# Performance work log

Hardware: AMD Instinct MI355X
Metric: run time of the kernel (lower is better)

## Reference

```python
import jax, jax.numpy as jnp
import numpy as np

NUM_HEADS = 16
THRESHOLD = 4e-4  # < 1/S so every softmax row keeps >=1 entry (classical path of grover_search_filter)


def setup_inputs() -> dict:
    key = jax.random.key(0)
    k0, k1, k2 = jax.random.split(key, 3)
    B, S, E = 4, 1024, 1024
    x = jax.random.normal(k0, (B, S, E), dtype=jnp.float32)
    Wqkv = jax.random.normal(k1, (3 * E, E), dtype=jnp.float32) * 0.02
    bqkv = jnp.zeros((3 * E,), dtype=jnp.float32)
    Wproj = jax.random.normal(k2, (E, E), dtype=jnp.float32) * 0.02
    bproj = jnp.zeros((E,), dtype=jnp.float32)
    return {"x": x, "Wqkv": Wqkv, "bqkv": bqkv, "Wproj": Wproj, "bproj": bproj}


def reference(x, Wqkv, bqkv, Wproj, bproj):
    B, S, E = x.shape
    H = NUM_HEADS
    D = E // H
    scale = D ** -0.5
    # qkv projection -> (3, B, H, S, D), matching torch permute(2,0,3,1,4)
    qkv = (x @ Wqkv.T + bqkv).reshape(B, S, 3, H, D).transpose(2, 0, 3, 1, 4)
    q, k, v = qkv[0], qkv[1], qkv[2]
    attn_logits = jnp.einsum("bhqd,bhkd->bhqk", q, k) * scale  # [B,H,S,S]
    attn_probs = jax.nn.softmax(attn_logits, axis=-1)
    # grover_search_filter: seq_len > 2**max_qubits -> classical threshold mask
    selected = attn_probs > THRESHOLD
    filtered_logits = jnp.where(selected, attn_logits, -jnp.inf)
    filtered_attn = jax.nn.softmax(filtered_logits, axis=-1)
    # dropout is identity in eval mode
    out = jnp.einsum("bhqk,bhkd->bhqd", filtered_attn, v)
    out = out.transpose(0, 2, 1, 3).reshape(B, S, E)
    out = out @ Wproj.T + bproj
    return out, filtered_attn
```

## Files before the change

kernel.cpp:

```cpp
#include <hip/hip_runtime.h>
#include <hip/hip_bf16.h>
#include <cstdint>


#define BB 4
#define SS 1024
#define EE 1024
#define HH 16
#define DD 64

typedef __attribute__((ext_vector_type(8))) short bf16x8;
typedef __attribute__((ext_vector_type(4))) float f32x4;

__global__ __launch_bounds__(256) void split_f32(
    const float* __restrict__ in, __hip_bfloat16* __restrict__ hi,
    __hip_bfloat16* __restrict__ lo, int n4) {
  int i = blockIdx.x * 256 + threadIdx.x;
  if (i >= n4) return;
  float4 v = ((const float4*)in)[i];
  float vv[4] = {v.x, v.y, v.z, v.w};
  __hip_bfloat16 h[4], l[4];
#pragma unroll
  for (int j = 0; j < 4; ++j) {
    h[j] = __float2bfloat16(vv[j]);
    l[j] = __float2bfloat16(vv[j] - __bfloat162float(h[j]));
  }
  ((ushort4*)hi)[i] = *(ushort4*)h;
  if (lo) ((ushort4*)lo)[i] = *(ushort4*)l;
}

template <int MODE>
__global__ __launch_bounds__(256) void gemm(
    const __hip_bfloat16* __restrict__ Ah, const __hip_bfloat16* __restrict__ Al,
    const __hip_bfloat16* __restrict__ Bh, const __hip_bfloat16* __restrict__ Bl,
    const float* __restrict__ Af, const float* __restrict__ bias,
    float* __restrict__ oF, __hip_bfloat16* __restrict__ o1,
    __hip_bfloat16* __restrict__ o2, __hip_bfloat16* __restrict__ o3,
    __hip_bfloat16* __restrict__ o4, __hip_bfloat16* __restrict__ o5,
    int M, int N, int K, int lda, int ldb, long long sA, long long sB) {
  constexpr bool SPLIT = (MODE == 0 || MODE == 1);
  constexpr bool AF32  = (MODE == 2);

  const int tid  = threadIdx.x;
  const int lane = tid & 63;
  const int wave = tid >> 6;
  const int wm   = (wave >> 1) * 64;
  const int wn   = (wave & 1) * 64;
  const int quad = lane >> 4;
  const int l15  = lane & 15;
  const int m0   = blockIdx.y * 128;
  const int n0   = blockIdx.x * 128;
  const long long zz = blockIdx.z;

  if (AF32) Af += zz * sA;
  else { Ah += zz * sA; if (SPLIT) Al += zz * sA; }
  Bh += zz * sB;
  if (SPLIT) Bl += zz * sB;

  __shared__ __align__(16) __hip_bfloat16 lds[(SPLIT ? 4 : 2) * 128 * 72];
  __hip_bfloat16* lAh = lds;
  __hip_bfloat16* lAl = SPLIT ? lds + 128 * 72 : nullptr;
  __hip_bfloat16* lBh = lds + (SPLIT ? 2 : 1) * 128 * 72;
  __hip_bfloat16* lBl = SPLIT ? lds + 3 * 128 * 72 : nullptr;

  f32x4 acc[4][4] = {};

  for (int k0 = 0; k0 < K; k0 += 64) {
#pragma unroll
    for (int it = 0; it < 4; ++it) {
      int flat = (it * 256 + tid) * 8;
      int row  = flat >> 6;
      int kk   = flat & 63;
      const bool mok = (m0 + row < M);
      const bool nok = (n0 + row < N);
      if (AF32) {
        float4 f0 = {0, 0, 0, 0}, f1 = {0, 0, 0, 0};
        if (mok) {
          const float* src = Af + (long long)(m0 + row) * lda + k0 + kk;
          f0 = *(const float4*)src;
          f1 = *(const float4*)(src + 4);
        }
        __hip_bfloat16 t[8];
        t[0] = __float2bfloat16(f0.x); t[1] = __float2bfloat16(f0.y);
        t[2] = __float2bfloat16(f0.z); t[3] = __float2bfloat16(f0.w);
        t[4] = __float2bfloat16(f1.x); t[5] = __float2bfloat16(f1.y);
        t[6] = __float2bfloat16(f1.z); t[7] = __float2bfloat16(f1.w);
        *(uint4*)&lAh[row * 72 + kk] = *(uint4*)t;
      } else {
        uint4 va = {0, 0, 0, 0};
        if (mok) va = *(const uint4*)(Ah + (long long)(m0 + row) * lda + k0 + kk);
        *(uint4*)&lAh[row * 72 + kk] = va;
        if (SPLIT) {
          uint4 vl = {0, 0, 0, 0};
          if (mok) vl = *(const uint4*)(Al + (long long)(m0 + row) * lda + k0 + kk);
          *(uint4*)&lAl[row * 72 + kk] = vl;
        }
      }
      uint4 vb = {0, 0, 0, 0};
      if (nok) vb = *(const uint4*)(Bh + (long long)(n0 + row) * ldb + k0 + kk);
      *(uint4*)&lBh[row * 72 + kk] = vb;
      if (SPLIT) {
        uint4 vbl = {0, 0, 0, 0};
        if (nok) vbl = *(const uint4*)(Bl + (long long)(n0 + row) * ldb + k0 + kk);
        *(uint4*)&lBl[row * 72 + kk] = vbl;
      }
    }
    __syncthreads();

#pragma unroll
    for (int ks = 0; ks < 64; ks += 32) {
      bf16x8 ah[4], bh[4], al[4], bl[4];
#pragma unroll
      for (int i = 0; i < 4; ++i) {
        int off = (wm + i * 16 + l15) * 72 + ks + quad * 8;
        ah[i] = *(const bf16x8*)&lAh[off];
        if (SPLIT) al[i] = *(const bf16x8*)&lAl[off];
      }
#pragma unroll
      for (int j = 0; j < 4; ++j) {
        int off = (wn + j * 16 + l15) * 72 + ks + quad * 8;
        bh[j] = *(const bf16x8*)&lBh[off];
        if (SPLIT) bl[j] = *(const bf16x8*)&lBl[off];
      }
#pragma unroll
      for (int i = 0; i < 4; ++i)
#pragma unroll
        for (int j = 0; j < 4; ++j) {
          if (SPLIT) {
            acc[i][j] = __builtin_amdgcn_mfma_f32_16x16x32_bf16(al[i], bh[j], acc[i][j], 0, 0, 0);
            acc[i][j] = __builtin_amdgcn_mfma_f32_16x16x32_bf16(ah[i], bl[j], acc[i][j], 0, 0, 0);
          }
          acc[i][j] = __builtin_amdgcn_mfma_f32_16x16x32_bf16(ah[i], bh[j], acc[i][j], 0, 0, 0);
        }
    }
    __syncthreads();
  }

#pragma unroll
  for (int i = 0; i < 4; ++i) {
#pragma unroll
    for (int j = 0; j < 4; ++j) {
#pragma unroll
      for (int r = 0; r < 4; ++r) {
        int m = m0 + wm + i * 16 + quad * 4 + r;
        int n = n0 + wn + j * 16 + l15;
        float v = acc[i][j][r];
        if (MODE == 0) {
          v += bias[n];
          int c = n >> 10, nn = n & 1023, h = nn >> 6, d = nn & 63;
          int b = m >> 10, s = m & 1023;
          long long idx = (((long long)(b * HH + h) * SS + s) << 6) + d;
          if (c == 0) {
            v *= 0.125f;
            __hip_bfloat16 hh = __float2bfloat16(v);
            o1[idx] = hh;
            o2[idx] = __float2bfloat16(v - __bfloat162float(hh));
          } else if (c == 1) {
            __hip_bfloat16 hh = __float2bfloat16(v);
            o3[idx] = hh;
            o4[idx] = __float2bfloat16(v - __bfloat162float(hh));
          } else {
            o5[(((long long)(b * HH + h) * DD + d) << 10) + s] = __float2bfloat16(v);
          }
        } else if (MODE == 1) {
          oF[zz * (SS * SS) + (long long)m * SS + n] = v * 0.125f;
        } else if (MODE == 2) {
          if (n < DD) {
            int b = (int)(zz >> 4), h = (int)(zz & 15);
            o1[(((long long)(b * SS + m)) << 10) + h * DD + n] = __float2bfloat16(v);
          }
        } else {
          oF[(long long)m * EE + n] = v + bias[n];
        }
      }
    }
  }
}

__device__ __forceinline__ float qg_max16(float v) {
#pragma unroll
  for (int o = 8; o > 0; o >>= 1) v = fmaxf(v, __shfl_xor(v, o));
  return v;
}
__device__ __forceinline__ float qg_sum16(float v) {
#pragma unroll
  for (int o = 8; o > 0; o >>= 1) v += __shfl_xor(v, o);
  return v;
}

__global__ __launch_bounds__(512, 4) void fused_attn(
    const __hip_bfloat16* __restrict__ qh, const __hip_bfloat16* __restrict__ ql,
    const __hip_bfloat16* __restrict__ kh, const __hip_bfloat16* __restrict__ kl,
    const __hip_bfloat16* __restrict__ vT, float* __restrict__ attn,
    __hip_bfloat16* __restrict__ ao) {
  const int tid  = threadIdx.x;
  const int lane = tid & 63;
  const int wave = tid >> 6;
  const int quad = lane >> 4;
  const int l15  = lane & 15;

  int id = blockIdx.x;
  const int q8 = gridDim.x >> 3;
  id = (id & 7) * q8 + (id >> 3);
  const int bh = id >> 5;
  const int q0 = (id & 31) * 32;

  const int brow = (bh >> 4) * SS;
  const int h    = bh & 15;
  const long long qbase = ((long long)bh * SS + q0) * DD;
  const long long kbase = (long long)bh * SS * DD;
  const long long vbase = (long long)bh * DD * SS;
  const long long abase = ((long long)bh * SS + q0) * SS;

  __shared__ __align__(16) __hip_bfloat16 Pl[32][1032];
  __shared__ float red[3][8][32];
  __shared__ float Obuf[4][32][17];

  bf16x8 aqh0[2], aqh1[2], aql0[2], aql1[2];
#pragma unroll
  for (int s = 0; s < 2; ++s) {
    const __hip_bfloat16* ph = qh + qbase + (s * 16 + l15) * DD + quad * 8;
    const __hip_bfloat16* pl = ql + qbase + (s * 16 + l15) * DD + quad * 8;
    aqh0[s] = *(const bf16x8*)(ph);
    aqh1[s] = *(const bf16x8*)(ph + 32);
    aql0[s] = *(const bf16x8*)(pl);
    aql1[s] = *(const bf16x8*)(pl + 32);
  }

  f32x4 acc0[8], acc1[8];
  const __hip_bfloat16* pkh0 = kh + kbase + (long long)(wave * 128 + l15) * DD + quad * 8;
  const __hip_bfloat16* pkl0 = kl + kbase + (long long)(wave * 128 + l15) * DD + quad * 8;
#pragma unroll
  for (int nt = 0; nt < 8; ++nt) {
    const __hip_bfloat16* pkh = pkh0 + nt * 16 * DD;
    const __hip_bfloat16* pkl = pkl0 + nt * 16 * DD;
    f32x4 a0 = {}, a1 = {};
    {
      bf16x8 b = *(const bf16x8*)(pkh);
      bf16x8 c = *(const bf16x8*)(pkl);
      __builtin_amdgcn_s_setprio(1);
      a0 = __builtin_amdgcn_mfma_f32_16x16x32_bf16(aql0[0], b, a0, 0, 0, 0);
      a1 = __builtin_amdgcn_mfma_f32_16x16x32_bf16(aql0[1], b, a1, 0, 0, 0);
      a0 = __builtin_amdgcn_mfma_f32_16x16x32_bf16(aqh0[0], c, a0, 0, 0, 0);
      a1 = __builtin_amdgcn_mfma_f32_16x16x32_bf16(aqh0[1], c, a1, 0, 0, 0);
      a0 = __builtin_amdgcn_mfma_f32_16x16x32_bf16(aqh0[0], b, a0, 0, 0, 0);
      a1 = __builtin_amdgcn_mfma_f32_16x16x32_bf16(aqh0[1], b, a1, 0, 0, 0);
      __builtin_amdgcn_s_setprio(0);
    }
    {
      bf16x8 b = *(const bf16x8*)(pkh + 32);
      bf16x8 c = *(const bf16x8*)(pkl + 32);
      __builtin_amdgcn_s_setprio(1);
      a0 = __builtin_amdgcn_mfma_f32_16x16x32_bf16(aql1[0], b, a0, 0, 0, 0);
      a1 = __builtin_amdgcn_mfma_f32_16x16x32_bf16(aql1[1], b, a1, 0, 0, 0);
      a0 = __builtin_amdgcn_mfma_f32_16x16x32_bf16(aqh1[0], c, a0, 0, 0, 0);
      a1 = __builtin_amdgcn_mfma_f32_16x16x32_bf16(aqh1[1], c, a1, 0, 0, 0);
      a0 = __builtin_amdgcn_mfma_f32_16x16x32_bf16(aqh1[0], b, a0, 0, 0, 0);
      a1 = __builtin_amdgcn_mfma_f32_16x16x32_bf16(aqh1[1], b, a1, 0, 0, 0);
      __builtin_amdgcn_s_setprio(0);
    }
    acc0[nt] = a0;
    acc1[nt] = a1;
  }

  {
    float mx0[4], mx1[4];
#pragma unroll
    for (int r = 0; r < 4; ++r) {
      float a = fmaxf(fmaxf(fmaxf(acc0[0][r], acc0[1][r]), fmaxf(acc0[2][r], acc0[3][r])),
                      fmaxf(fmaxf(acc0[4][r], acc0[5][r]), fmaxf(acc0[6][r], acc0[7][r])));
      mx0[r] = qg_max16(a);
      float b = fmaxf(fmaxf(fmaxf(acc1[0][r], acc1[1][r]), fmaxf(acc1[2][r], acc1[3][r])),
                      fmaxf(fmaxf(acc1[4][r], acc1[5][r]), fmaxf(acc1[6][r], acc1[7][r])));
      mx1[r] = qg_max16(b);
    }
    if (l15 == 0) {
#pragma unroll
      for (int r = 0; r < 4; ++r) {
        red[0][wave][quad * 4 + r]      = mx0[r];
        red[0][wave][16 + quad * 4 + r] = mx1[r];
      }
    }
  }
  __syncthreads();
  float m0[4], m1[4];
#pragma unroll
  for (int r = 0; r < 4; ++r) {
    const int q = quad * 4 + r;
    m0[r] = fmaxf(fmaxf(fmaxf(red[0][0][q], red[0][1][q]), fmaxf(red[0][2][q], red[0][3][q])),
                  fmaxf(fmaxf(red[0][4][q], red[0][5][q]), fmaxf(red[0][6][q], red[0][7][q])));
    m1[r] = fmaxf(fmaxf(fmaxf(red[0][0][16 + q], red[0][1][16 + q]), fmaxf(red[0][2][16 + q], red[0][3][16 + q])),
                  fmaxf(fmaxf(red[0][4][16 + q], red[0][5][16 + q]), fmaxf(red[0][6][16 + q], red[0][7][16 + q])));
  }

  {
    float z0[4] = {0.f, 0.f, 0.f, 0.f}, z1[4] = {0.f, 0.f, 0.f, 0.f};
#pragma unroll
    for (int nt = 0; nt < 8; ++nt)
#pragma unroll
      for (int r = 0; r < 4; ++r) {
        float e0 = expf(acc0[nt][r] - m0[r]);
        acc0[nt][r] = e0; z0[r] += e0;
        float e1 = expf(acc1[nt][r] - m1[r]);
        acc1[nt][r] = e1; z1[r] += e1;
      }
#pragma unroll
    for (int r = 0; r < 4; ++r) { z0[r] = qg_sum16(z0[r]); z1[r] = qg_sum16(z1[r]); }
    if (l15 == 0) {
#pragma unroll
      for (int r = 0; r < 4; ++r) {
        red[1][wave][quad * 4 + r]      = z0[r];
        red[1][wave][16 + quad * 4 + r] = z1[r];
      }
    }
  }
  __syncthreads();
  float c0[4], c1[4];
#pragma unroll
  for (int r = 0; r < 4; ++r) {
    const int q = quad * 4 + r;
    const float Z0 = ((red[1][0][q] + red[1][1][q]) + (red[1][2][q] + red[1][3][q])) +
                     ((red[1][4][q] + red[1][5][q]) + (red[1][6][q] + red[1][7][q]));
    const float Z1 = ((red[1][0][16 + q] + red[1][1][16 + q]) + (red[1][2][16 + q] + red[1][3][16 + q])) +
                     ((red[1][4][16 + q] + red[1][5][16 + q]) + (red[1][6][16 + q] + red[1][7][16 + q]));
    c0[r] = 4e-4f * Z0;
    c1[r] = 4e-4f * Z1;
  }

  {
    float s0[4] = {0.f, 0.f, 0.f, 0.f}, s1[4] = {0.f, 0.f, 0.f, 0.f};
#pragma unroll
    for (int nt = 0; nt < 8; ++nt)
#pragma unroll
      for (int r = 0; r < 4; ++r) {
        if (acc0[nt][r] > c0[r]) s0[r] += acc0[nt][r];
        if (acc1[nt][r] > c1[r]) s1[r] += acc1[nt][r];
      }
#pragma unroll
    for (int r = 0; r < 4; ++r) { s0[r] = qg_sum16(s0[r]); s1[r] = qg_sum16(s1[r]); }
    if (l15 == 0) {
#pragma unroll
      for (int r = 0; r < 4; ++r) {
        red[2][wave][quad * 4 + r]      = s0[r];
        red[2][wave][16 + quad * 4 + r] = s1[r];
      }
    }
  }
  __syncthreads();
  float rinv0[4], rinv1[4];
#pragma unroll
  for (int r = 0; r < 4; ++r) {
    const int q = quad * 4 + r;
    const float Zs0 = ((red[2][0][q] + red[2][1][q]) + (red[2][2][q] + red[2][3][q])) +
                      ((red[2][4][q] + red[2][5][q]) + (red[2][6][q] + red[2][7][q]));
    const float Zs1 = ((red[2][0][16 + q] + red[2][1][16 + q]) + (red[2][2][16 + q] + red[2][3][16 + q])) +
                      ((red[2][4][16 + q] + red[2][5][16 + q]) + (red[2][6][16 + q] + red[2][7][16 + q]));
    rinv0[r] = 1.0f / Zs0;
    rinv1[r] = 1.0f / Zs1;
  }

#pragma unroll
  for (int nt = 0; nt < 8; ++nt) {
    const int k = wave * 128 + nt * 16 + l15;
#pragma unroll
    for (int r = 0; r < 4; ++r) {
      const int q = quad * 4 + r;
      const float e0 = acc0[nt][r];
      const float p0 = (e0 > c0[r]) ? e0 * rinv0[r] : 0.f;
      attn[abase + (long long)q * SS + k] = p0;
      Pl[q][k] = __float2bfloat16(p0);
      const float e1 = acc1[nt][r];
      const float p1 = (e1 > c1[r]) ? e1 * rinv1[r] : 0.f;
      attn[abase + (long long)(16 + q) * SS + k] = p1;
      Pl[16 + q][k] = __float2bfloat16(p1);
    }
  }
  __syncthreads();

  const int d0  = (wave & 3) * 16;
  const int kh2 = (wave >> 2) * 512;
  f32x4 oA0 = {}, oA1 = {}, oB0 = {}, oB1 = {};
  const __hip_bfloat16* pv  = vT + vbase + (long long)(d0 + l15) * SS + kh2 + quad * 8;
  const __hip_bfloat16* pp0 = &Pl[l15][kh2] + quad * 8;
  const __hip_bfloat16* pp1 = &Pl[16 + l15][kh2] + quad * 8;
#pragma unroll
  for (int ks = 0; ks < 16; ks += 2) {
    bf16x8 v0  = *(const bf16x8*)(pv + ks * 32);
    bf16x8 v1  = *(const bf16x8*)(pv + (ks + 1) * 32);
    bf16x8 a00 = *(const bf16x8*)(pp0 + ks * 32);
    bf16x8 a01 = *(const bf16x8*)(pp0 + (ks + 1) * 32);
    bf16x8 a10 = *(const bf16x8*)(pp1 + ks * 32);
    bf16x8 a11 = *(const bf16x8*)(pp1 + (ks + 1) * 32);
    __builtin_amdgcn_s_setprio(1);
    oA0 = __builtin_amdgcn_mfma_f32_16x16x32_bf16(a00, v0, oA0, 0, 0, 0);
    oB0 = __builtin_amdgcn_mfma_f32_16x16x32_bf16(a10, v0, oB0, 0, 0, 0);
    oA1 = __builtin_amdgcn_mfma_f32_16x16x32_bf16(a01, v1, oA1, 0, 0, 0);
    oB1 = __builtin_amdgcn_mfma_f32_16x16x32_bf16(a11, v1, oB1, 0, 0, 0);
    __builtin_amdgcn_s_setprio(0);
  }
  float oS0[4], oS1[4];
#pragma unroll
  for (int r = 0; r < 4; ++r) { oS0[r] = oA0[r] + oA1[r]; oS1[r] = oB0[r] + oB1[r]; }

  if (wave >= 4) {
#pragma unroll
    for (int r = 0; r < 4; ++r) {
      Obuf[wave & 3][quad * 4 + r][l15]      = oS0[r];
      Obuf[wave & 3][16 + quad * 4 + r][l15] = oS1[r];
    }
  }
  __syncthreads();
  if (wave < 4) {
#pragma unroll
    for (int r = 0; r < 4; ++r) {
      const int qA = q0 + quad * 4 + r;
      const int qB = qA + 16;
      const float vA = oS0[r] + Obuf[wave][quad * 4 + r][l15];
      const float vB = oS1[r] + Obuf[wave][16 + quad * 4 + r][l15];
      ao[((long long)(brow + qA)) * EE + h * DD + d0 + l15] = __float2bfloat16(vA);
      ao[((long long)(brow + qB)) * EE + h * DD + d0 + l15] = __float2bfloat16(vB);
    }
  }
}

extern "C" void kernel_launch(void* const* d_in, const int* in_sizes, int n_in,
                              void* d_out, int out_size, void* d_ws, size_t ws_size,
                              hipStream_t stream) {
  const float* x     = (const float*)d_in[0];
  const float* Wqkv  = (const float*)d_in[1];
  const float* bqkv  = (const float*)d_in[2];
  const float* Wproj = (const float*)d_in[3];
  const float* bproj = (const float*)d_in[4];

  float* out   = (float*)d_out;
  float* attnF = out + (size_t)BB * SS * EE;

  const size_t M1 = 1024 * 1024;
  __hip_bfloat16* w = (__hip_bfloat16*)d_ws;

  if (ws_size >= (size_t)80 * 1024 * 1024) {
    __hip_bfloat16 *xh = w, *xl = xh + 4 * M1;
    __hip_bfloat16 *Wqh = xl + 4 * M1, *Wql = Wqh + 3 * M1, *Wph = Wql + 3 * M1;
    __hip_bfloat16 *qh = Wph + M1, *ql = qh + 4 * M1, *kh = ql + 4 * M1, *kl = kh + 4 * M1;
    __hip_bfloat16 *vT = kl + 4 * M1, *ao = vT + 4 * M1;

    split_f32<<<4096, 256, 0, stream>>>(x, xh, xl, 1024 * 1024);
    split_f32<<<3072, 256, 0, stream>>>(Wqkv, Wqh, Wql, 768 * 1024);
    split_f32<<<1024, 256, 0, stream>>>(Wproj, Wph, nullptr, 256 * 1024);

    gemm<0><<<dim3(24, 32, 1), 256, 0, stream>>>(
        xh, xl, Wqh, Wql, nullptr, bqkv, nullptr, qh, ql, kh, kl, vT,
        4096, 3072, 1024, 1024, 1024, 0LL, 0LL);
    fused_attn<<<dim3(BB * HH * 32), 512, 0, stream>>>(
        qh, ql, kh, kl, vT, attnF, ao);
    gemm<3><<<dim3(8, 32, 1), 256, 0, stream>>>(
        ao, nullptr, Wph, nullptr, nullptr, bproj, out, nullptr, nullptr, nullptr, nullptr, nullptr,
        4096, 1024, 1024, 1024, 1024, 0LL, 0LL);
    return;
  }

  __hip_bfloat16 *Wqh = w, *Wql = Wqh + 3 * M1, *Wph = Wql + 3 * M1;
  __hip_bfloat16 *xh = Wph + M1, *xl = xh + M1;
  __hip_bfloat16 *qh = xl + M1, *ql = qh + M1, *kh = ql + M1, *kl = kh + M1;
  __hip_bfloat16 *vT = kl + M1, *ao = vT + M1;

  split_f32<<<3072, 256, 0, stream>>>(Wqkv, Wqh, Wql, 768 * 1024);
  split_f32<<<1024, 256, 0, stream>>>(Wproj, Wph, nullptr, 256 * 1024);

  for (int b = 0; b < BB; ++b) {
    const float* xb   = x + (size_t)b * SS * EE;
    float* attnb      = attnF + (size_t)b * HH * SS * SS;
    float* outb       = out + (size_t)b * SS * EE;

    split_f32<<<1024, 256, 0, stream>>>(xb, xh, xl, 256 * 1024);
    gemm<0><<<dim3(24, 8, 1), 256, 0, stream>>>(
        xh, xl, Wqh, Wql, nullptr, bqkv, nullptr, qh, ql, kh, kl, vT,
        1024, 3072, 1024, 1024, 1024, 0LL, 0LL);
    fused_attn<<<dim3(HH * 32), 512, 0, stream>>>(
        qh, ql, kh, kl, vT, attnb, ao);
    gemm<3><<<dim3(8, 8, 1), 256, 0, stream>>>(
        ao, nullptr, Wph, nullptr, nullptr, bproj, outb, nullptr, nullptr, nullptr, nullptr, nullptr,
        1024, 1024, 1024, 1024, 1024, 0LL, 0LL);
  }
}
```

Before: 670.4 us.

## Fuse x bf16 split into QKV GEMM and merge weight split kernels

The QKV GEMM now reads fp32 x directly and splits it into hi/lo bf16 while staging tiles into LDS. This removes the separate split pass and its 16 MB of hi/lo bf16 intermediates for x. The weight operands are no longer staged through LDS and are loaded straight from global memory into registers, and the two weight split kernels are merged into one launch. The direct B loads are strided per lane and uncoalesced, and they are re-read by each wave, which may raise memory traffic in exchange for less LDS use.

After: 649.9 us. 3.1% less time.

```diff
diff --git a/kernel.cpp b/kernel.cpp
--- a/kernel.cpp
+++ b/kernel.cpp
@@ -12,35 +12,39 @@
 typedef __attribute__((ext_vector_type(8))) short bf16x8;
 typedef __attribute__((ext_vector_type(4))) float f32x4;
 
-__global__ __launch_bounds__(256) void split_f32(
-    const float* __restrict__ in, __hip_bfloat16* __restrict__ hi,
-    __hip_bfloat16* __restrict__ lo, int n4) {
+__global__ __launch_bounds__(256) void split_w(
+    const float* __restrict__ Wqkv, const float* __restrict__ Wproj,
+    __hip_bfloat16* __restrict__ Wqh, __hip_bfloat16* __restrict__ Wql,
+    __hip_bfloat16* __restrict__ Wph) {
   int i = blockIdx.x * 256 + threadIdx.x;
-  if (i >= n4) return;
-  float4 v = ((const float4*)in)[i];
-  float vv[4] = {v.x, v.y, v.z, v.w};
-  __hip_bfloat16 h[4], l[4];
-#pragma unroll
-  for (int j = 0; j < 4; ++j) {
-    h[j] = __float2bfloat16(vv[j]);
-    l[j] = __float2bfloat16(vv[j] - __bfloat162float(h[j]));
-  }
-  ((ushort4*)hi)[i] = *(ushort4*)h;
-  if (lo) ((ushort4*)lo)[i] = *(ushort4*)l;
-}
-
-template <int MODE>
-__global__ __launch_bounds__(256) void gemm(
-    const __hip_bfloat16* __restrict__ Ah, const __hip_bfloat16* __restrict__ Al,
-    const __hip_bfloat16* __restrict__ Bh, const __hip_bfloat16* __restrict__ Bl,
-    const float* __restrict__ Af, const float* __restrict__ bias,
-    float* __restrict__ oF, __hip_bfloat16* __restrict__ o1,
-    __hip_bfloat16* __restrict__ o2, __hip_bfloat16* __restrict__ o3,
-    __hip_bfloat16* __restrict__ o4, __hip_bfloat16* __restrict__ o5,
-    int M, int N, int K, int lda, int ldb, long long sA, long long sB) {
-  constexpr bool SPLIT = (MODE == 0 || MODE == 1);
-  constexpr bool AF32  = (MODE == 2);
-
+  const int NQ4 = 768 * 1024;
+  if (i < NQ4) {
+    float4 v = ((const float4*)Wqkv)[i];
+    float vv[4] = {v.x, v.y, v.z, v.w};
+    __hip_bfloat16 h[4], l[4];
+#pragma unroll
+    for (int j = 0; j < 4; ++j) {
+      h[j] = __float2bfloat16(vv[j]);
+      l[j] = __float2bfloat16(vv[j] - __bfloat162float(h[j]));
+    }
+    ((ushort4*)Wqh)[i] = *(ushort4*)h;
+    ((ushort4*)Wql)[i] = *(ushort4*)l;
+  } else {
+    int j4 = i - NQ4;
+    float4 v = ((const float4*)Wproj)[j4];
+    __hip_bfloat16 h[4];
+    h[0] = __float2bfloat16(v.x); h[1] = __float2bfloat16(v.y);
+    h[2] = __float2bfloat16(v.z); h[3] = __float2bfloat16(v.w);
+    ((ushort4*)Wph)[j4] = *(ushort4*)h;
+  }
+}
+
+__global__ __launch_bounds__(256) void gemm_qkv(
+    const float* __restrict__ X, const __hip_bfloat16* __restrict__ Wh,
+    const __hip_bfloat16* __restrict__ Wl, const float* __restrict__ bias,
+    __hip_bfloat16* __restrict__ o1, __hip_bfloat16* __restrict__ o2,
+    __hip_bfloat16* __restrict__ o3, __hip_bfloat16* __restrict__ o4,
+    __hip_bfloat16* __restrict__ o5, int M) {
   const int tid  = threadIdx.x;
   const int lane = tid & 63;
   const int wave = tid >> 6;
@@ -50,86 +54,56 @@
   const int l15  = lane & 15;
   const int m0   = blockIdx.y * 128;
   const int n0   = blockIdx.x * 128;
-  const long long zz = blockIdx.z;
-
-  if (AF32) Af += zz * sA;
-  else { Ah += zz * sA; if (SPLIT) Al += zz * sA; }
-  Bh += zz * sB;
-  if (SPLIT) Bl += zz * sB;
-
-  __shared__ __align__(16) __hip_bfloat16 lds[(SPLIT ? 4 : 2) * 128 * 72];
-  __hip_bfloat16* lAh = lds;
-  __hip_bfloat16* lAl = SPLIT ? lds + 128 * 72 : nullptr;
-  __hip_bfloat16* lBh = lds + (SPLIT ? 2 : 1) * 128 * 72;
-  __hip_bfloat16* lBl = SPLIT ? lds + 3 * 128 * 72 : nullptr;
+
+  __shared__ __align__(16) __hip_bfloat16 lAh[128 * 72];
+  __shared__ __align__(16) __hip_bfloat16 lAl[128 * 72];
 
   f32x4 acc[4][4] = {};
-
-  for (int k0 = 0; k0 < K; k0 += 64) {
+  const __hip_bfloat16* pBh = Wh + (long long)(n0 + wn + l15) * 1024 + quad * 8;
+  const __hip_bfloat16* pBl = Wl + (long long)(n0 + wn + l15) * 1024 + quad * 8;
+
+  for (int k0 = 0; k0 < 1024; k0 += 64) {
 #pragma unroll
     for (int it = 0; it < 4; ++it) {
       int flat = (it * 256 + tid) * 8;
       int row  = flat >> 6;
       int kk   = flat & 63;
-      const bool mok = (m0 + row < M);
-      const bool nok = (n0 + row < N);
-      if (AF32) {
-        float4 f0 = {0, 0, 0, 0}, f1 = {0, 0, 0, 0};
-        if (mok) {
-          const float* src = Af + (long long)(m0 + row) * lda + k0 + kk;
-          f0 = *(const float4*)src;
-          f1 = *(const float4*)(src + 4);
-        }
-        __hip_bfloat16 t[8];
-        t[0] = __float2bfloat16(f0.x); t[1] = __float2bfloat16(f0.y);
-        t[2] = __float2bfloat16(f0.z); t[3] = __float2bfloat16(f0.w);
-        t[4] = __float2bfloat16(f1.x); t[5] = __float2bfloat16(f1.y);
-        t[6] = __float2bfloat16(f1.z); t[7] = __float2bfloat16(f1.w);
-        *(uint4*)&lAh[row * 72 + kk] = *(uint4*)t;
-      } else {
-        uint4 va = {0, 0, 0, 0};
-        if (mok) va = *(const uint4*)(Ah + (long long)(m0 + row) * lda + k0 + kk);
-        *(uint4*)&lAh[row * 72 + kk] = va;
-        if (SPLIT) {
-          uint4 vl = {0, 0, 0, 0};
-          if (mok) vl = *(const uint4*)(Al + (long long)(m0 + row) * lda + k0 + kk);
-          *(uint4*)&lAl[row * 72 + kk] = vl;
-        }
-      }
-      uint4 vb = {0, 0, 0, 0};
-      if (nok) vb = *(const uint4*)(Bh + (long long)(n0 + row) * ldb + k0 + kk);
-      *(uint4*)&lBh[row * 72 + kk] = vb;
-      if (SPLIT) {
-        uint4 vbl = {0, 0, 0, 0};
-        if (nok) vbl = *(const uint4*)(Bl + (long long)(n0 + row) * ldb + k0 + kk);
-        *(uint4*)&lBl[row * 72 + kk] = vbl;
-      }
+      const float* src = X + (long long)(m0 + row) * 1024 + k0 + kk;
+      float4 f0 = *(const float4*)src;
+      float4 f1 = *(const float4*)(src + 4);
+      float vv[8] = {f0.x, f0.y, f0.z, f0.w, f1.x, f1.y, f1.z, f1.w};
+      __hip_bfloat16 t[8], u[8];
+#pragma unroll
+      for (int j2 = 0; j2 < 8; ++j2) {
+        t[j2] = __float2bfloat16(vv[j2]);
+        u[j2] = __float2bfloat16(vv[j2] - __bfloat162float(t[j2]));
+      }
+      *(uint4*)&lAh[row * 72 + kk] = *(uint4*)t;
+      *(uint4*)&lAl[row * 72 + kk] = *(uint4*)u;
     }
     __syncthreads();
 
 #pragma unroll
     for (int ks = 0; ks < 64; ks += 32) {
-      bf16x8 ah[4], bh[4], al[4], bl[4];
+      bf16x8 ah[4], al[4], bh[4], bl[4];
 #pragma unroll
       for (int i = 0; i < 4; ++i) {
         int off = (wm + i * 16 + l15) * 72 + ks + quad * 8;
         ah[i] = *(const bf16x8*)&lAh[off];
-        if (SPLIT) al[i] = *(const bf16x8*)&lAl[off];
+        al[i] = *(const bf16x8*)&lAl[off];
       }
 #pragma unroll
       for (int j = 0; j < 4; ++j) {
-        int off = (wn + j * 16 + l15) * 72 + ks + quad * 8;
-        bh[j] = *(const bf16x8*)&lBh[off];
-        if (SPLIT) bl[j] = *(const bf16x8*)&lBl[off];
+        const long long boff = (long long)j * 16 * 1024 + k0 + ks;
+        bh[j] = *(const bf16x8*)(pBh + boff);
+        bl[j] = *(const bf16x8*)(pBl + boff);
       }
 #pragma unroll
       for (int i = 0; i < 4; ++i)
 #pragma unroll
         for (int j = 0; j < 4; ++j) {
-          if (SPLIT) {
-            acc[i][j] = __builtin_amdgcn_mfma_f32_16x16x32_bf16(al[i], bh[j], acc[i][j], 0, 0, 0);
-            acc[i][j] = __builtin_amdgcn_mfma_f32_16x16x32_bf16(ah[i], bl[j], acc[i][j], 0, 0, 0);
-          }
+          acc[i][j] = __builtin_amdgcn_mfma_f32_16x16x32_bf16(al[i], bh[j], acc[i][j], 0, 0, 0);
+          acc[i][j] = __builtin_amdgcn_mfma_f32_16x16x32_bf16(ah[i], bl[j], acc[i][j], 0, 0, 0);
           acc[i][j] = __builtin_amdgcn_mfma_f32_16x16x32_bf16(ah[i], bh[j], acc[i][j], 0, 0, 0);
         }
     }
@@ -144,37 +118,87 @@
       for (int r = 0; r < 4; ++r) {
         int m = m0 + wm + i * 16 + quad * 4 + r;
         int n = n0 + wn + j * 16 + l15;
-        float v = acc[i][j][r];
-        if (MODE == 0) {
-          v += bias[n];
-          int c = n >> 10, nn = n & 1023, h = nn >> 6, d = nn & 63;
-          int b = m >> 10, s = m & 1023;
-          long long idx = (((long long)(b * HH + h) * SS + s) << 6) + d;
-          if (c == 0) {
-            v *= 0.125f;
-            __hip_bfloat16 hh = __float2bfloat16(v);
-            o1[idx] = hh;
-            o2[idx] = __float2bfloat16(v - __bfloat162float(hh));
-          } else if (c == 1) {
-            __hip_bfloat16 hh = __float2bfloat16(v);
-            o3[idx] = hh;
-            o4[idx] = __float2bfloat16(v - __bfloat162float(hh));
-          } else {
-            o5[(((long long)(b * HH + h) * DD + d) << 10) + s] = __float2bfloat16(v);
-          }
-        } else if (MODE == 1) {
-          oF[zz * (SS * SS) + (long long)m * SS + n] = v * 0.125f;
-        } else if (MODE == 2) {
-          if (n < DD) {
-            int b = (int)(zz >> 4), h = (int)(zz & 15);
-            o1[(((long long)(b * SS + m)) << 10) + h * DD + n] = __float2bfloat16(v);
-          }
+        float v = acc[i][j][r] + bias[n];
+        int c = n >> 10, nn = n & 1023, h = nn >> 6, d = nn & 63;
+        int b = m >> 10, s = m & 1023;
+        long long idx = (((long long)(b * HH + h) * SS + s) << 6) + d;
+        if (c == 0) {
+          v *= 0.125f;
+          __hip_bfloat16 hh = __float2bfloat16(v);
+          o1[idx] = hh;
+          o2[idx] = __float2bfloat16(v - __bfloat162float(hh));
+        } else if (c == 1) {
+          __hip_bfloat16 hh = __float2bfloat16(v);
+          o3[idx] = hh;
+          o4[idx] = __float2bfloat16(v - __bfloat162float(hh));
         } else {
-          oF[(long long)m * EE + n] = v + bias[n];
+          o5[(((long long)(b * HH + h) * DD + d) << 10) + s] = __float2bfloat16(v);
         }
       }
     }
   }
+}
+
+__global__ __launch_bounds__(256) void gemm_out(
+    const __hip_bfloat16* __restrict__ Ah, const __hip_bfloat16* __restrict__ Bh,
+    const float* __restrict__ bias, float* __restrict__ oF, int M) {
+  const int tid  = threadIdx.x;
+  const int lane = tid & 63;
+  const int wave = tid >> 6;
+  const int wm   = (wave >> 1) * 64;
+  const int wn   = (wave & 1) * 64;
+  const int quad = lane >> 4;
+  const int l15  = lane & 15;
+  const int m0   = blockIdx.y * 128;
+  const int n0   = blockIdx.x * 128;
+
+  __shared__ __align__(16) __hip_bfloat16 lds[2 * 128 * 72];
+  __hip_bfloat16* lA = lds;
+  __hip_bfloat16* lB = lds + 128 * 72;
+
+  f32x4 acc[4][4] = {};
+
+  for (int k0 = 0; k0 < 1024; k0 += 64) {
+#pragma unroll
+    for (int it = 0; it < 4; ++it) {
+      int flat = (it * 256 + tid) * 8;
+      int row  = flat >> 6;
+      int kk   = flat & 63;
+      uint4 va = *(const uint4*)(Ah + (long long)(m0 + row) * 1024 + k0 + kk);
+      *(uint4*)&lA[row * 72 + kk] = va;
+      uint4 vb = *(const uint4*)(Bh + (long long)(n0 + row) * 1024 + k0 + kk);
+      *(uint4*)&lB[row * 72 + kk] = vb;
+    }
+    __syncthreads();
+
+#pragma unroll
+    for (int ks = 0; ks < 64; ks += 32) {
+      bf16x8 ah[4], bh[4];
+#pragma unroll
+      for (int i = 0; i < 4; ++i)
+        ah[i] = *(const bf16x8*)&lA[(wm + i * 16 + l15) * 72 + ks + quad * 8];
+#pragma unroll
+      for (int j = 0; j < 4; ++j)
+        bh[j] = *(const bf16x8*)&lB[(wn + j * 16 + l15) * 72 + ks + quad * 8];
+#pragma unroll
+      for (int i = 0; i < 4; ++i)
+#pragma unroll
+        for (int j = 0; j < 4; ++j)
+          acc[i][j] = __builtin_amdgcn_mfma_f32_16x16x32_bf16(ah[i], bh[j], acc[i][j], 0, 0, 0);
+    }
+    __syncthreads();
+  }
+
+#pragma unroll
+  for (int i = 0; i < 4; ++i)
+#pragma unroll
+    for (int j = 0; j < 4; ++j)
+#pragma unroll
+      for (int r = 0; r < 4; ++r) {
+        int m = m0 + wm + i * 16 + quad * 4 + r;
+        int n = n0 + wn + j * 16 + l15;
+        oF[(long long)m * EE + n] = acc[i][j][r] + bias[n];
+      }
 }
 
 __device__ __forceinline__ float qg_max16(float v) {
@@ -439,47 +463,34 @@
   __hip_bfloat16* w = (__hip_bfloat16*)d_ws;
 
   if (ws_size >= (size_t)80 * 1024 * 1024) {
-    __hip_bfloat16 *xh = w, *xl = xh + 4 * M1;
-    __hip_bfloat16 *Wqh = xl + 4 * M1, *Wql = Wqh + 3 * M1, *Wph = Wql + 3 * M1;
+    __hip_bfloat16 *Wqh = w, *Wql = Wqh + 3 * M1, *Wph = Wql + 3 * M1;
     __hip_bfloat16 *qh = Wph + M1, *ql = qh + 4 * M1, *kh = ql + 4 * M1, *kl = kh + 4 * M1;
     __hip_bfloat16 *vT = kl + 4 * M1, *ao = vT + 4 * M1;
 
-    split_f32<<<4096, 256, 0, stream>>>(x, xh, xl, 1024 * 1024);
-    split_f32<<<3072, 256, 0, stream>>>(Wqkv, Wqh, Wql, 768 * 1024);
-    split_f32<<<1024, 256, 0, stream>>>(Wproj, Wph, nullptr, 256 * 1024);
-
-    gemm<0><<<dim3(24, 32, 1), 256, 0, stream>>>(
-        xh, xl, Wqh, Wql, nullptr, bqkv, nullptr, qh, ql, kh, kl, vT,
-        4096, 3072, 1024, 1024, 1024, 0LL, 0LL);
+    split_w<<<4096, 256, 0, stream>>>(Wqkv, Wproj, Wqh, Wql, Wph);
+    gemm_qkv<<<dim3(24, 32), 256, 0, stream>>>(
+        x, Wqh, Wql, bqkv, qh, ql, kh, kl, vT, 4096);
     fused_attn<<<dim3(BB * HH * 32), 512, 0, stream>>>(
         qh, ql, kh, kl, vT, attnF, ao);
-    gemm<3><<<dim3(8, 32, 1), 256, 0, stream>>>(
-        ao, nullptr, Wph, nullptr, nullptr, bproj, out, nullptr, nullptr, nullptr, nullptr, nullptr,
-        4096, 1024, 1024, 1024, 1024, 0LL, 0LL);
+    gemm_out<<<dim3(8, 32), 256, 0, stream>>>(ao, Wph, bproj, out, 4096);
     return;
   }
 
   __hip_bfloat16 *Wqh = w, *Wql = Wqh + 3 * M1, *Wph = Wql + 3 * M1;
-  __hip_bfloat16 *xh = Wph + M1, *xl = xh + M1;
-  __hip_bfloat16 *qh = xl + M1, *ql = qh + M1, *kh = ql + M1, *kl = kh + M1;
+  __hip_bfloat16 *qh = Wph + M1, *ql = qh + M1, *kh = ql + M1, *kl = kh + M1;
   __hip_bfloat16 *vT = kl + M1, *ao = vT + M1;
 
-  split_f32<<<3072, 256, 0, stream>>>(Wqkv, Wqh, Wql, 768 * 1024);
-  split_f32<<<1024, 256, 0, stream>>>(Wproj, Wph, nullptr, 256 * 1024);
+  split_w<<<4096, 256, 0, stream>>>(Wqkv, Wproj, Wqh, Wql, Wph);
 
   for (int b = 0; b < BB; ++b) {
     const float* xb   = x + (size_t)b * SS * EE;
     float* attnb      = attnF + (size_t)b * HH * SS * SS;
     float* outb       = out + (size_t)b * SS * EE;
 
-    split_f32<<<1024, 256, 0, stream>>>(xb, xh, xl, 256 * 1024);
-    gemm<0><<<dim3(24, 8, 1), 256, 0, stream>>>(
-        xh, xl, Wqh, Wql, nullptr, bqkv, nullptr, qh, ql, kh, kl, vT,
-        1024, 3072, 1024, 1024, 1024, 0LL, 0LL);
+    gemm_qkv<<<dim3(24, 8), 256, 0, stream>>>(
+        xb, Wqh, Wql, bqkv, qh, ql, kh, kl, vT, 1024);
     fused_attn<<<dim3(HH * 32), 512, 0, stream>>>(
         qh, ql, kh, kl, vT, attnb, ao);
-    gemm<3><<<dim3(8, 8, 1), 256, 0, stream>>>(
-        ao, nullptr, Wph, nullptr, nullptr, bproj, outb, nullptr, nullptr, nullptr, nullptr, nullptr,
-        1024, 1024, 1024, 1024, 1024, 0LL, 0LL);
-  }
-}
+    gemm_out<<<dim3(8, 8), 256, 0, stream>>>(ao, Wph, bproj, outb, 1024);
+  }
+}
```
